# Kernel optimization log

Hardware: AMD Instinct MI355X
Metric: run time of the kernel (lower is better)

The kernel has to match this reference:

```python
import jax, jax.numpy as jnp
import numpy as np

B, L, D = 4, 2048, 512
H = 8
DK = 512 // H  # 64
DV = 512 // H  # 64
TEMP = float(np.power(DK, 0.5))
LN_EPS = 1e-5


def setup_inputs() -> dict:
    key = jax.random.key(0)
    ks = jax.random.split(key, 12)
    s = 0.02
    return {
        "q": jax.random.normal(ks[0], (B, L, D), jnp.float32),
        "k": jax.random.normal(ks[1], (B, L, D), jnp.float32),
        "v": jax.random.normal(ks[2], (B, L, D), jnp.float32),
        "mask": jax.random.randint(ks[3], (B, L, L), 0, 2, jnp.int32),
        "wq_w": jax.random.normal(ks[4], (H * DK, D), jnp.float32) * s,
        "wq_b": jnp.zeros((H * DK,), jnp.float32),
        "wv_w": jax.random.normal(ks[5], (H * DV, D), jnp.float32) * s,
        "wv_b": jnp.zeros((H * DV,), jnp.float32),
        "fc_w": jax.random.normal(ks[6], (D, H * DV), jnp.float32) * s,
        "fc_b": jnp.zeros((D,), jnp.float32),
        "ln_g": jnp.ones((D,), jnp.float32),
        "ln_b": jnp.zeros((D,), jnp.float32),
    }


def reference(q, k, v, mask, wq_w, wq_b, wv_w, wv_b, fc_w, fc_b, ln_g, ln_b):
    residual = q
    # NOTE: source module projects k with w_qs (bug preserved faithfully)
    qh = (q @ wq_w.T + wq_b).reshape(B, L, H, DK).transpose(0, 2, 1, 3)  # bhld
    kh = (k @ wq_w.T + wq_b).reshape(B, L, H, DK).transpose(0, 2, 1, 3)
    vh = (v @ wv_w.T + wv_b).reshape(B, L, H, DV).transpose(0, 2, 1, 3)
    attn = jnp.einsum("bhqd,bhkd->bhqk", qh / TEMP, kh)
    attn = jnp.where(mask[:, None, :, :] == 1, -1e9, attn)
    attn = jax.nn.softmax(attn, axis=-1)
    out = jnp.einsum("bhqk,bhkd->bhqd", attn, vh)  # (B, H, L, DV)
    # faithful buffer reinterpretation: .view(n_head, sz_b, L, DV)
    out = out.reshape(H, B, L, DV).transpose(0, 2, 1, 3).reshape(B, L, H * DV)
    out = out @ fc_w.T + fc_b
    x = out + residual
    mu = jnp.mean(x, axis=-1, keepdims=True)
    var = jnp.mean(jnp.square(x - mu), axis=-1, keepdims=True)
    y = (x - mu) / jnp.sqrt(var + LN_EPS) * ln_g + ln_b
    return (y, attn)
```

## Files before the change

kernel.cpp:

```cpp
#include <hip/hip_runtime.h>

#define NB 4
#define NL 2048
#define ND 512
#define NH 8
#define NTOK (NB * NL)

constexpr float LN_EPS = 1e-5f;

typedef __attribute__((ext_vector_type(8))) short bf16x8;
typedef __attribute__((ext_vector_type(4))) float f32x4;

static __device__ __forceinline__ unsigned short f2bf(float f) {
  unsigned u = __builtin_bit_cast(unsigned, f);
  unsigned r = (u + 0x7fffu + ((u >> 16) & 1u)) >> 16;
  return (unsigned short)r;
}

static __device__ __forceinline__ uint2 pk4(const float4 f) {
  uint2 r;
  r.x = (unsigned)f2bf(f.x) | ((unsigned)f2bf(f.y) << 16);
  r.y = (unsigned)f2bf(f.z) | ((unsigned)f2bf(f.w) << 16);
  return r;
}

__global__ __launch_bounds__(256) void cvt3_bf16(const float* __restrict__ s0,
                                                 const float* __restrict__ s1,
                                                 const float* __restrict__ s2,
                                                 unsigned short* __restrict__ d0,
                                                 unsigned short* __restrict__ d1,
                                                 unsigned short* __restrict__ d2) {
  const float* s = (blockIdx.y == 0) ? s0 : (blockIdx.y == 1) ? s1 : s2;
  unsigned short* d = (blockIdx.y == 0) ? d0 : (blockIdx.y == 1) ? d1 : d2;
  const size_t i = ((size_t)blockIdx.x * 256 + threadIdx.x) * 8;
  const float4 a = *(const float4*)&s[i];
  const float4 b = *(const float4*)&s[i + 4];
  uint4 o;
  const uint2 lo = pk4(a), hi = pk4(b);
  o.x = lo.x; o.y = lo.y; o.z = hi.x; o.w = hi.y;
  *(uint4*)&d[i] = o;
}

__global__ __launch_bounds__(256) void pack_mask(const int* __restrict__ mask,
                                                 unsigned long long* __restrict__ mpk) {
  const int w = threadIdx.x >> 6, lane = threadIdx.x & 63;
  const size_t g = (size_t)blockIdx.x * 4 + w;
  const int m = mask[g * 64 + lane];
  const unsigned long long bits = __ballot(m == 1);
  if (lane == 0) mpk[g] = bits;
}

#define BF16_GEMM_PRELUDE                                                      \
  __shared__ unsigned short As[64 * 72];                                       \
  __shared__ unsigned short Bs[64 * 72];                                       \
  const int tid = threadIdx.x;                                                 \
  const int w = tid >> 6;                                                      \
  const int lane = tid & 63;                                                   \
  const int quad = lane >> 4, l15 = lane & 15;                                 \
  const int m0 = blockIdx.x * 64, n0 = blockIdx.y * 64;                        \
  const int srow = tid >> 2;                                                   \
  const int scol = (tid & 3) * 16;                                             \
  f32x4 acc[4];                                                                \
  acc[0] = acc[1] = acc[2] = acc[3] = (f32x4){0.f, 0.f, 0.f, 0.f};

#define BF16_GEMM_STEP(ap, bp)                                                 \
  do {                                                                         \
    const uint4 a0 = *(const uint4*)((ap));                                    \
    const uint4 a1 = *(const uint4*)((ap) + 8);                                \
    const uint4 b0 = *(const uint4*)((bp));                                    \
    const uint4 b1 = *(const uint4*)((bp) + 8);                                \
    __syncthreads();                                                           \
    *(uint4*)&As[srow * 72 + scol] = a0;                                       \
    *(uint4*)&As[srow * 72 + scol + 8] = a1;                                   \
    *(uint4*)&Bs[srow * 72 + scol] = b0;                                       \
    *(uint4*)&Bs[srow * 72 + scol + 8] = b1;                                   \
    __syncthreads();                                                           \
    _Pragma("unroll") for (int ks = 0; ks < 2; ++ks) {                         \
      const bf16x8 af = *(const bf16x8*)&As[(w * 16 + l15) * 72 + ks * 32 + quad * 8]; \
      _Pragma("unroll") for (int nt = 0; nt < 4; ++nt) {                       \
        const bf16x8 bfr = *(const bf16x8*)&Bs[(nt * 16 + l15) * 72 + ks * 32 + quad * 8]; \
        acc[nt] = __builtin_amdgcn_mfma_f32_16x16x32_bf16(af, bfr, acc[nt], 0, 0, 0); \
      }                                                                        \
    }                                                                          \
  } while (0)

__global__ __launch_bounds__(256) void gemm_qk_mfma(const unsigned short* __restrict__ X,
                                                    const unsigned short* __restrict__ W,
                                                    const float* __restrict__ bias,
                                                    unsigned short* __restrict__ out,
                                                    float scale) {
  BF16_GEMM_PRELUDE
  for (int k0 = 0; k0 < 512; k0 += 64) {
    const unsigned short* ap = X + (size_t)(m0 + srow) * ND + k0 + scol;
    const unsigned short* bp = W + (size_t)(n0 + srow) * ND + k0 + scol;
    BF16_GEMM_STEP(ap, bp);
  }
  const int hh = n0 >> 6;
  __syncthreads();
#pragma unroll
  for (int nt = 0; nt < 4; ++nt) {
    const float b = bias[n0 + nt * 16 + l15];
#pragma unroll
    for (int r = 0; r < 4; ++r)
      As[(w * 16 + quad * 4 + r) * 72 + nt * 16 + l15] = f2bf((acc[nt][r] + b) * scale);
  }
  __syncthreads();
  const int tok = m0 + srow;
  const int bb = tok >> 11, l = tok & 2047;
  unsigned short* orow = out + (((size_t)bb * NH + hh) * NL + l) * 64;
  *(uint4*)&orow[scol] = *(const uint4*)&As[srow * 72 + scol];
  *(uint4*)&orow[scol + 8] = *(const uint4*)&As[srow * 72 + scol + 8];
}

__global__ __launch_bounds__(256) void gemm_v_mfma_t(const unsigned short* __restrict__ X,
                                                     const unsigned short* __restrict__ W,
                                                     const float* __restrict__ bias,
                                                     unsigned short* __restrict__ outT) {
  BF16_GEMM_PRELUDE
  for (int k0 = 0; k0 < 512; k0 += 64) {
    const unsigned short* ap = X + (size_t)(m0 + srow) * ND + k0 + scol;
    const unsigned short* bp = W + (size_t)(n0 + srow) * ND + k0 + scol;
    BF16_GEMM_STEP(ap, bp);
  }
  const int hh = n0 >> 6;
  __syncthreads();
#pragma unroll
  for (int nt = 0; nt < 4; ++nt) {
    const float b = bias[n0 + nt * 16 + l15];
#pragma unroll
    for (int r = 0; r < 4; ++r)
      As[(nt * 16 + l15) * 72 + w * 16 + quad * 4 + r] = f2bf(acc[nt][r] + b);
  }
  __syncthreads();
  const int bb = m0 >> 11, l0 = m0 & 2047;
  unsigned short* orow = outT + (((size_t)bb * NH + hh) * 64 + srow) * NL + l0;
  *(uint4*)&orow[scol] = *(const uint4*)&As[srow * 72 + scol];
  *(uint4*)&orow[scol + 8] = *(const uint4*)&As[srow * 72 + scol + 8];
}

__global__ __launch_bounds__(256) void attn_mfma(const unsigned short* __restrict__ qh,
                                                 const unsigned short* __restrict__ kh,
                                                 const unsigned short* __restrict__ vT,
                                                 const unsigned long long* __restrict__ mpk,
                                                 float* __restrict__ attn,
                                                 unsigned short* __restrict__ ao) {
  const int b = blockIdx.z, h = blockIdx.y, q0 = blockIdx.x * 64;
  const int bh = b * NH + h;
  __shared__ unsigned short Ks[64 * 72];
  __shared__ unsigned short Vt[64 * 72];
  __shared__ unsigned short Ps[4 * 16 * 72];
  const int tid = threadIdx.x;
  const int w = tid >> 6, lane = tid & 63;
  const int quad = lane >> 4, l15 = lane & 15;

  const size_t qoff = ((size_t)bh * NL + q0 + w * 16 + l15) * 64 + quad * 8;
  const bf16x8 aq0 = *(const bf16x8*)(qh + qoff);
  const bf16x8 aq1 = *(const bf16x8*)(qh + qoff + 32);

  const int srow = tid >> 2;
  const int scol = (tid & 3) * 16;

  const size_t mrowq = ((size_t)b * NL + q0 + w * 16 + quad * 4) * 32;

  float rinv[4] = {0.f, 0.f, 0.f, 0.f};
  unsigned int mbits[16];
#pragma unroll
  for (int i = 0; i < 16; ++i) mbits[i] = 0;

  for (int kt = 0; kt < 32; ++kt) {
    const unsigned short* kg = kh + ((size_t)bh * NL + kt * 64 + srow) * 64 + scol;
    const uint4 k0 = *(const uint4*)kg;
    const uint4 k1 = *(const uint4*)(kg + 8);
    unsigned long long mq[4];
#pragma unroll
    for (int r = 0; r < 4; ++r) mq[r] = mpk[mrowq + (size_t)r * 32 + kt];
    __syncthreads();
    *(uint4*)&Ks[srow * 72 + scol] = k0;
    *(uint4*)&Ks[srow * 72 + scol + 8] = k1;
    __syncthreads();
    f32x4 s[4];
#pragma unroll
    for (int nt = 0; nt < 4; ++nt) {
      const bf16x8 b0 = *(const bf16x8*)&Ks[(nt * 16 + l15) * 72 + quad * 8];
      const bf16x8 b1 = *(const bf16x8*)&Ks[(nt * 16 + l15) * 72 + 32 + quad * 8];
      f32x4 acc = {0.f, 0.f, 0.f, 0.f};
      acc = __builtin_amdgcn_mfma_f32_16x16x32_bf16(aq0, b0, acc, 0, 0, 0);
      acc = __builtin_amdgcn_mfma_f32_16x16x32_bf16(aq1, b1, acc, 0, 0, 0);
      s[nt] = acc;
    }
    unsigned int mb = 0;
#pragma unroll
    for (int r = 0; r < 4; ++r) {
      const unsigned long long t = mq[r] >> l15;
      mb |= ((unsigned)t & 1u) << (0 + r);
      mb |= (((unsigned)t >> 16) & 1u) << (4 + r);
      mb |= (((unsigned)(t >> 32)) & 1u) << (8 + r);
      mb |= (((unsigned)(t >> 48)) & 1u) << (12 + r);
    }
#pragma unroll
    for (int r = 0; r < 4; ++r) {
#pragma unroll
      for (int nt = 0; nt < 4; ++nt) {
        const float e = ((mb >> (nt * 4 + r)) & 1u) ? 0.f : __expf(s[nt][r]);
        rinv[r] += e;
      }
    }
    mbits[kt >> 1] |= mb << ((kt & 1) * 16);
  }
#pragma unroll
  for (int r = 0; r < 4; ++r) {
    float v = rinv[r];
    v += __shfl_xor(v, 1);
    v += __shfl_xor(v, 2);
    v += __shfl_xor(v, 4);
    v += __shfl_xor(v, 8);
    rinv[r] = 1.0f / v;
  }

  f32x4 oacc[4];
#pragma unroll
  for (int nt = 0; nt < 4; ++nt) oacc[nt] = (f32x4){0.f, 0.f, 0.f, 0.f};

  for (int kt = 0; kt < 32; ++kt) {
    const unsigned short* kg = kh + ((size_t)bh * NL + kt * 64 + srow) * 64 + scol;
    const unsigned short* vg = vT + ((size_t)bh * 64 + srow) * NL + kt * 64 + scol;
    const uint4 k0 = *(const uint4*)kg;
    const uint4 k1 = *(const uint4*)(kg + 8);
    const uint4 v0 = *(const uint4*)vg;
    const uint4 v1 = *(const uint4*)(vg + 8);
    __syncthreads();
    *(uint4*)&Ks[srow * 72 + scol] = k0;
    *(uint4*)&Ks[srow * 72 + scol + 8] = k1;
    *(uint4*)&Vt[srow * 72 + scol] = v0;
    *(uint4*)&Vt[srow * 72 + scol + 8] = v1;
    __syncthreads();
    f32x4 s[4];
#pragma unroll
    for (int nt = 0; nt < 4; ++nt) {
      const bf16x8 b0 = *(const bf16x8*)&Ks[(nt * 16 + l15) * 72 + quad * 8];
      const bf16x8 b1 = *(const bf16x8*)&Ks[(nt * 16 + l15) * 72 + 32 + quad * 8];
      f32x4 acc = {0.f, 0.f, 0.f, 0.f};
      acc = __builtin_amdgcn_mfma_f32_16x16x32_bf16(aq0, b0, acc, 0, 0, 0);
      acc = __builtin_amdgcn_mfma_f32_16x16x32_bf16(aq1, b1, acc, 0, 0, 0);
      s[nt] = acc;
    }
    const unsigned int mb = mbits[kt >> 1] >> ((kt & 1) * 16);
#pragma unroll
    for (int r = 0; r < 4; ++r) {
      const int q = q0 + w * 16 + quad * 4 + r;
      float* arow = attn + ((size_t)bh * NL + q) * NL + kt * 64;
      unsigned short* prow = &Ps[(w * 16 + quad * 4 + r) * 72];
#pragma unroll
      for (int nt = 0; nt < 4; ++nt) {
        float e = ((mb >> (nt * 4 + r)) & 1u) ? 0.f : __expf(s[nt][r]) * rinv[r];
        arow[nt * 16 + l15] = e;
        prow[nt * 16 + l15] = f2bf(e);
      }
    }
    const bf16x8 pa0 = *(const bf16x8*)&Ps[(w * 16 + l15) * 72 + quad * 8];
    const bf16x8 pa1 = *(const bf16x8*)&Ps[(w * 16 + l15) * 72 + 32 + quad * 8];
#pragma unroll
    for (int nt = 0; nt < 4; ++nt) {
      const bf16x8 vb0 = *(const bf16x8*)&Vt[(nt * 16 + l15) * 72 + quad * 8];
      const bf16x8 vb1 = *(const bf16x8*)&Vt[(nt * 16 + l15) * 72 + 32 + quad * 8];
      oacc[nt] = __builtin_amdgcn_mfma_f32_16x16x32_bf16(pa0, vb0, oacc[nt], 0, 0, 0);
      oacc[nt] = __builtin_amdgcn_mfma_f32_16x16x32_bf16(pa1, vb1, oacc[nt], 0, 0, 0);
    }
  }
#pragma unroll
  for (int nt = 0; nt < 4; ++nt)
#pragma unroll
    for (int r = 0; r < 4; ++r)
      Ps[(w * 16 + quad * 4 + r) * 72 + nt * 16 + l15] = f2bf(oacc[nt][r]);
  const int erow = lane >> 2;
  const int ecol = (lane & 3) * 16;
  unsigned short* orow = ao + (((size_t)bh * NL + q0 + w * 16 + erow) * 64) + ecol;
  *(uint4*)&orow[0] = *(const uint4*)&Ps[(w * 16 + erow) * 72 + ecol];
  *(uint4*)&orow[8] = *(const uint4*)&Ps[(w * 16 + erow) * 72 + ecol + 8];
}

__global__ __launch_bounds__(256) void fc_gather_mfma(const unsigned short* __restrict__ AO,
                                                      const unsigned short* __restrict__ W,
                                                      const float* __restrict__ bias,
                                                      const float* __restrict__ resid,
                                                      float* __restrict__ Xout) {
  BF16_GEMM_PRELUDE
  const int nrow = m0 + srow;
  const int b_out = nrow >> 11;
  const int l_out = nrow & 2047;
  const int h2 = b_out * 2 + (l_out >> 10);
  const int q2base = (l_out & 1023) << 1;
  for (int k0 = 0; k0 < 512; k0 += 64) {
    const int q2 = q2base | ((k0 >> 8) & 1);
    const int b2 = (k0 >> 6) & 3;
    const unsigned short* ap = AO + ((size_t)(h2 * 4 + b2) * NL + q2) * 64 + scol;
    const unsigned short* bp = W + (size_t)(n0 + srow) * ND + k0 + scol;
    BF16_GEMM_STEP(ap, bp);
  }
#pragma unroll
  for (int nt = 0; nt < 4; ++nt) {
    const float b = bias[n0 + nt * 16 + l15];
#pragma unroll
    for (int r = 0; r < 4; ++r) {
      const int row = m0 + w * 16 + quad * 4 + r;
      const float rv = resid[(size_t)row * ND + n0 + nt * 16 + l15];
      Xout[(size_t)row * ND + n0 + nt * 16 + l15] = acc[nt][r] + b + rv;
    }
  }
}

__global__ __launch_bounds__(64) void layernorm_k(const float* __restrict__ x,
                                                  const float* __restrict__ g,
                                                  const float* __restrict__ bta,
                                                  float* __restrict__ y) {
  const int n = blockIdx.x;
  const int lane = threadIdx.x;
  const float* row = x + (size_t)n * ND;
  const float4 a = *(const float4*)&row[lane * 8];
  const float4 c = *(const float4*)&row[lane * 8 + 4];
  float s = a.x + a.y + a.z + a.w + c.x + c.y + c.z + c.w;
  float sq = a.x * a.x + a.y * a.y + a.z * a.z + a.w * a.w +
             c.x * c.x + c.y * c.y + c.z * c.z + c.w * c.w;
#pragma unroll
  for (int off = 32; off; off >>= 1) {
    s += __shfl_down(s, off);
    sq += __shfl_down(sq, off);
  }
  s = __shfl(s, 0);
  sq = __shfl(sq, 0);
  const float mu = s * (1.f / 512.f);
  const float var = sq * (1.f / 512.f) - mu * mu;
  const float rstd = rsqrtf(var + LN_EPS);
  float* yo = y + (size_t)n * ND;
  const int c0 = lane * 8;
  float4 o1, o2;
  o1.x = (a.x - mu) * rstd * g[c0 + 0] + bta[c0 + 0];
  o1.y = (a.y - mu) * rstd * g[c0 + 1] + bta[c0 + 1];
  o1.z = (a.z - mu) * rstd * g[c0 + 2] + bta[c0 + 2];
  o1.w = (a.w - mu) * rstd * g[c0 + 3] + bta[c0 + 3];
  o2.x = (c.x - mu) * rstd * g[c0 + 4] + bta[c0 + 4];
  o2.y = (c.y - mu) * rstd * g[c0 + 5] + bta[c0 + 5];
  o2.z = (c.z - mu) * rstd * g[c0 + 6] + bta[c0 + 6];
  o2.w = (c.w - mu) * rstd * g[c0 + 7] + bta[c0 + 7];
  *(float4*)&yo[c0] = o1;
  *(float4*)&yo[c0 + 4] = o2;
}

extern "C" void kernel_launch(void* const* d_in, const int* in_sizes, int n_in,
                              void* d_out, int out_size, void* d_ws, size_t ws_size,
                              hipStream_t stream) {
  const float* q = (const float*)d_in[0];
  const float* k = (const float*)d_in[1];
  const float* v = (const float*)d_in[2];
  const int* mask = (const int*)d_in[3];
  const float* wq_w = (const float*)d_in[4];
  const float* wq_b = (const float*)d_in[5];
  const float* wv_w = (const float*)d_in[6];
  const float* wv_b = (const float*)d_in[7];
  const float* fc_w = (const float*)d_in[8];
  const float* fc_b = (const float*)d_in[9];
  const float* ln_g = (const float*)d_in[10];
  const float* ln_b = (const float*)d_in[11];

  float* y = (float*)d_out;
  float* attn = y + (size_t)NTOK * ND;

  const size_t SZ = (size_t)NTOK * ND;
  const size_t WSZ = (size_t)ND * ND;
  unsigned short* qhb = (unsigned short*)d_ws;
  unsigned short* khb = qhb + SZ;
  unsigned short* vTb = khb + SZ;
  unsigned short* aob = vTb + SZ;
  unsigned short* qb = aob + SZ;
  unsigned short* kb = qb + SZ;
  unsigned short* vb = kb + SZ;
  float* xx = (float*)(vb + SZ);
  unsigned short* wqb = (unsigned short*)(xx + SZ);
  unsigned short* wvb = wqb + WSZ;
  unsigned short* fcwb = wvb + WSZ;
  unsigned long long* mpk = (unsigned long long*)(fcwb + WSZ);

  cvt3_bf16<<<dim3(SZ / 2048, 3), 256, 0, stream>>>(q, k, v, qb, kb, vb);
  cvt3_bf16<<<dim3(WSZ / 2048, 3), 256, 0, stream>>>(wq_w, wv_w, fc_w, wqb, wvb, fcwb);
  pack_mask<<<(NB * NL * 32) / 4, 256, 0, stream>>>(mask, mpk);

  const dim3 gproj(NTOK / 64, ND / 64);
  gemm_qk_mfma<<<gproj, 256, 0, stream>>>(qb, wqb, wq_b, qhb, 0.125f);
  gemm_qk_mfma<<<gproj, 256, 0, stream>>>(kb, wqb, wq_b, khb, 1.0f);
  gemm_v_mfma_t<<<gproj, 256, 0, stream>>>(vb, wvb, wv_b, vTb);
  attn_mfma<<<dim3(NL / 64, NH, NB), 256, 0, stream>>>(qhb, khb, vTb, mpk, attn, aob);
  fc_gather_mfma<<<gproj, 256, 0, stream>>>(aob, fcwb, fc_b, q, xx);
  layernorm_k<<<NTOK, 64, 0, stream>>>(xx, ln_g, ln_b, y);
}
```

Baseline: 822.0 us.

## Double-buffer 128-row GEMM tiles, prefetch K/V in attention, use exp2

```diff
diff --git a/kernel.cpp b/kernel.cpp
--- a/kernel.cpp
+++ b/kernel.cpp
@@ -50,38 +50,49 @@
   if (lane == 0) mpk[g] = bits;
 }
 
-#define BF16_GEMM_PRELUDE                                                      \
-  __shared__ unsigned short As[64 * 72];                                       \
-  __shared__ unsigned short Bs[64 * 72];                                       \
+#define GEMM128_PRELUDE                                                        \
+  __shared__ unsigned short As[2][128 * 72];                                   \
+  __shared__ unsigned short Bs[2][64 * 72];                                    \
   const int tid = threadIdx.x;                                                 \
   const int w = tid >> 6;                                                      \
   const int lane = tid & 63;                                                   \
   const int quad = lane >> 4, l15 = lane & 15;                                 \
-  const int m0 = blockIdx.x * 64, n0 = blockIdx.y * 64;                        \
-  const int srow = tid >> 2;                                                   \
-  const int scol = (tid & 3) * 16;                                             \
-  f32x4 acc[4];                                                                \
-  acc[0] = acc[1] = acc[2] = acc[3] = (f32x4){0.f, 0.f, 0.f, 0.f};
-
-#define BF16_GEMM_STEP(ap, bp)                                                 \
-  do {                                                                         \
-    const uint4 a0 = *(const uint4*)((ap));                                    \
-    const uint4 a1 = *(const uint4*)((ap) + 8);                                \
-    const uint4 b0 = *(const uint4*)((bp));                                    \
-    const uint4 b1 = *(const uint4*)((bp) + 8);                                \
-    __syncthreads();                                                           \
-    *(uint4*)&As[srow * 72 + scol] = a0;                                       \
-    *(uint4*)&As[srow * 72 + scol + 8] = a1;                                   \
-    *(uint4*)&Bs[srow * 72 + scol] = b0;                                       \
-    *(uint4*)&Bs[srow * 72 + scol + 8] = b1;                                   \
-    __syncthreads();                                                           \
+  const int m0 = blockIdx.x * 128, n0 = blockIdx.y * 64;                       \
+  const int arow = tid >> 1;                                       \
+  const int acol = (tid & 1) * 32;                     \
+  const int brow = tid >> 2;                                        \
+  const int bcol = (tid & 3) * 16;                                             \
+  f32x4 acc[2][4];                                                             \
+  _Pragma("unroll") for (int mr = 0; mr < 2; ++mr)                             \
+  _Pragma("unroll") for (int nt = 0; nt < 4; ++nt)                             \
+    acc[mr][nt] = (f32x4){0.f, 0.f, 0.f, 0.f};                                 \
+  uint4 ar[4], br[2];
+
+#define GEMM128_STORE_LDS(buf)                                                 \
+  do {                                                                         \
+    _Pragma("unroll") for (int j = 0; j < 4; ++j)                              \
+      *(uint4*)&As[buf][arow * 72 + acol + j * 8] = ar[j];                     \
+    *(uint4*)&Bs[buf][brow * 72 + bcol] = br[0];                               \
+    *(uint4*)&Bs[buf][brow * 72 + bcol + 8] = br[1];                           \
+  } while (0)
+
+#define GEMM128_COMPUTE(buf)                                                   \
+  do {                                                                         \
     _Pragma("unroll") for (int ks = 0; ks < 2; ++ks) {                         \
-      const bf16x8 af = *(const bf16x8*)&As[(w * 16 + l15) * 72 + ks * 32 + quad * 8]; \
+      const bf16x8 af0 = *(const bf16x8*)&As[buf][(w * 32 + l15) * 72 + ks * 32 + quad * 8]; \
+      const bf16x8 af1 = *(const bf16x8*)&As[buf][(w * 32 + 16 + l15) * 72 + ks * 32 + quad * 8]; \
       _Pragma("unroll") for (int nt = 0; nt < 4; ++nt) {                       \
-        const bf16x8 bfr = *(const bf16x8*)&Bs[(nt * 16 + l15) * 72 + ks * 32 + quad * 8]; \
-        acc[nt] = __builtin_amdgcn_mfma_f32_16x16x32_bf16(af, bfr, acc[nt], 0, 0, 0); \
+        const bf16x8 bfr = *(const bf16x8*)&Bs[buf][(nt * 16 + l15) * 72 + ks * 32 + quad * 8]; \
+        acc[0][nt] = __builtin_amdgcn_mfma_f32_16x16x32_bf16(af0, bfr, acc[0][nt], 0, 0, 0); \
+        acc[1][nt] = __builtin_amdgcn_mfma_f32_16x16x32_bf16(af1, bfr, acc[1][nt], 0, 0, 0); \
       }                                                                        \
     }                                                                          \
+  } while (0)
+
+#define GEMM128_LOADB(k0)                                                      \
+  do {                                                                         \
+    br[0] = *(const uint4*)&W[(size_t)(n0 + brow) * ND + (k0) + bcol];         \
+    br[1] = *(const uint4*)&W[(size_t)(n0 + brow) * ND + (k0) + bcol + 8];     \
   } while (0)
 
 __global__ __launch_bounds__(256) void gemm_qk_mfma(const unsigned short* __restrict__ X,
@@ -89,53 +100,90 @@
                                                     const float* __restrict__ bias,
                                                     unsigned short* __restrict__ out,
                                                     float scale) {
-  BF16_GEMM_PRELUDE
-  for (int k0 = 0; k0 < 512; k0 += 64) {
-    const unsigned short* ap = X + (size_t)(m0 + srow) * ND + k0 + scol;
-    const unsigned short* bp = W + (size_t)(n0 + srow) * ND + k0 + scol;
-    BF16_GEMM_STEP(ap, bp);
-  }
+  GEMM128_PRELUDE
+#define LOADA_QK(k0)                                                           \
+  do {                                                                         \
+    _Pragma("unroll") for (int j = 0; j < 4; ++j)                              \
+      ar[j] = *(const uint4*)&X[(size_t)(m0 + arow) * ND + (k0) + acol + j * 8]; \
+  } while (0)
+  LOADA_QK(0);
+  GEMM128_LOADB(0);
+#pragma unroll
+  for (int t = 0; t < 8; ++t) {
+    const int buf = t & 1;
+    GEMM128_STORE_LDS(buf);
+    __syncthreads();
+    if (t < 7) {
+      LOADA_QK((t + 1) * 64);
+      GEMM128_LOADB((t + 1) * 64);
+    }
+    GEMM128_COMPUTE(buf);
+  }
+#undef LOADA_QK
   const int hh = n0 >> 6;
+#pragma unroll
+  for (int mr = 0; mr < 2; ++mr)
+#pragma unroll
+    for (int nt = 0; nt < 4; ++nt) {
+      const float b = bias[n0 + nt * 16 + l15];
+#pragma unroll
+      for (int r = 0; r < 4; ++r)
+        As[0][(w * 32 + mr * 16 + quad * 4 + r) * 72 + nt * 16 + l15] =
+            f2bf((acc[mr][nt][r] + b) * scale);
+    }
   __syncthreads();
-#pragma unroll
-  for (int nt = 0; nt < 4; ++nt) {
-    const float b = bias[n0 + nt * 16 + l15];
-#pragma unroll
-    for (int r = 0; r < 4; ++r)
-      As[(w * 16 + quad * 4 + r) * 72 + nt * 16 + l15] = f2bf((acc[nt][r] + b) * scale);
-  }
-  __syncthreads();
-  const int tok = m0 + srow;
+  const int tok = m0 + arow;
   const int bb = tok >> 11, l = tok & 2047;
   unsigned short* orow = out + (((size_t)bb * NH + hh) * NL + l) * 64;
-  *(uint4*)&orow[scol] = *(const uint4*)&As[srow * 72 + scol];
-  *(uint4*)&orow[scol + 8] = *(const uint4*)&As[srow * 72 + scol + 8];
+#pragma unroll
+  for (int j = 0; j < 4; ++j)
+    *(uint4*)&orow[acol + j * 8] = *(const uint4*)&As[0][arow * 72 + acol + j * 8];
 }
 
 __global__ __launch_bounds__(256) void gemm_v_mfma_t(const unsigned short* __restrict__ X,
                                                      const unsigned short* __restrict__ W,
                                                      const float* __restrict__ bias,
                                                      unsigned short* __restrict__ outT) {
-  BF16_GEMM_PRELUDE
-  for (int k0 = 0; k0 < 512; k0 += 64) {
-    const unsigned short* ap = X + (size_t)(m0 + srow) * ND + k0 + scol;
-    const unsigned short* bp = W + (size_t)(n0 + srow) * ND + k0 + scol;
-    BF16_GEMM_STEP(ap, bp);
-  }
+  GEMM128_PRELUDE
+#define LOADA_V(k0)                                                            \
+  do {                                                                         \
+    _Pragma("unroll") for (int j = 0; j < 4; ++j)                              \
+      ar[j] = *(const uint4*)&X[(size_t)(m0 + arow) * ND + (k0) + acol + j * 8]; \
+  } while (0)
+  LOADA_V(0);
+  GEMM128_LOADB(0);
+#pragma unroll
+  for (int t = 0; t < 8; ++t) {
+    const int buf = t & 1;
+    GEMM128_STORE_LDS(buf);
+    __syncthreads();
+    if (t < 7) {
+      LOADA_V((t + 1) * 64);
+      GEMM128_LOADB((t + 1) * 64);
+    }
+    GEMM128_COMPUTE(buf);
+  }
+#undef LOADA_V
   const int hh = n0 >> 6;
-  __syncthreads();
-#pragma unroll
-  for (int nt = 0; nt < 4; ++nt) {
-    const float b = bias[n0 + nt * 16 + l15];
-#pragma unroll
-    for (int r = 0; r < 4; ++r)
-      As[(nt * 16 + l15) * 72 + w * 16 + quad * 4 + r] = f2bf(acc[nt][r] + b);
-  }
+  unsigned short* T = &As[0][0];
+#pragma unroll
+  for (int mr = 0; mr < 2; ++mr)
+#pragma unroll
+    for (int nt = 0; nt < 4; ++nt) {
+      const float b = bias[n0 + nt * 16 + l15];
+#pragma unroll
+      for (int r = 0; r < 4; ++r)
+        T[(nt * 16 + l15) * 136 + (w * 32 + mr * 16 + quad * 4 + r)] =
+            f2bf(acc[mr][nt][r] + b);
+    }
   __syncthreads();
   const int bb = m0 >> 11, l0 = m0 & 2047;
-  unsigned short* orow = outT + (((size_t)bb * NH + hh) * 64 + srow) * NL + l0;
-  *(uint4*)&orow[scol] = *(const uint4*)&As[srow * 72 + scol];
-  *(uint4*)&orow[scol + 8] = *(const uint4*)&As[srow * 72 + scol + 8];
+  const int d = tid >> 2;
+  const int lcol = (tid & 3) * 32;
+  unsigned short* orow = outT + (((size_t)bb * NH + hh) * 64 + d) * NL + l0;
+#pragma unroll
+  for (int j = 0; j < 4; ++j)
+    *(uint4*)&orow[lcol + j * 8] = *(const uint4*)&T[d * 136 + lcol + j * 8];
 }
 
 __global__ __launch_bounds__(256) void attn_mfma(const unsigned short* __restrict__ qh,
@@ -160,52 +208,58 @@
   const int srow = tid >> 2;
   const int scol = (tid & 3) * 16;
 
+  const size_t kbase = ((size_t)bh * NL + srow) * 64 + scol;
+  const size_t vbase = ((size_t)bh * 64 + srow) * NL + scol;
   const size_t mrowq = ((size_t)b * NL + q0 + w * 16 + quad * 4) * 32;
 
   float rinv[4] = {0.f, 0.f, 0.f, 0.f};
-  unsigned int mbits[16];
-#pragma unroll
-  for (int i = 0; i < 16; ++i) mbits[i] = 0;
-
-  for (int kt = 0; kt < 32; ++kt) {
-    const unsigned short* kg = kh + ((size_t)bh * NL + kt * 64 + srow) * 64 + scol;
-    const uint4 k0 = *(const uint4*)kg;
-    const uint4 k1 = *(const uint4*)(kg + 8);
-    unsigned long long mq[4];
-#pragma unroll
-    for (int r = 0; r < 4; ++r) mq[r] = mpk[mrowq + (size_t)r * 32 + kt];
-    __syncthreads();
-    *(uint4*)&Ks[srow * 72 + scol] = k0;
-    *(uint4*)&Ks[srow * 72 + scol + 8] = k1;
-    __syncthreads();
-    f32x4 s[4];
-#pragma unroll
-    for (int nt = 0; nt < 4; ++nt) {
-      const bf16x8 b0 = *(const bf16x8*)&Ks[(nt * 16 + l15) * 72 + quad * 8];
-      const bf16x8 b1 = *(const bf16x8*)&Ks[(nt * 16 + l15) * 72 + 32 + quad * 8];
-      f32x4 acc = {0.f, 0.f, 0.f, 0.f};
-      acc = __builtin_amdgcn_mfma_f32_16x16x32_bf16(aq0, b0, acc, 0, 0, 0);
-      acc = __builtin_amdgcn_mfma_f32_16x16x32_bf16(aq1, b1, acc, 0, 0, 0);
-      s[nt] = acc;
-    }
-    unsigned int mb = 0;
-#pragma unroll
-    for (int r = 0; r < 4; ++r) {
-      const unsigned long long t = mq[r] >> l15;
-      mb |= ((unsigned)t & 1u) << (0 + r);
-      mb |= (((unsigned)t >> 16) & 1u) << (4 + r);
-      mb |= (((unsigned)(t >> 32)) & 1u) << (8 + r);
-      mb |= (((unsigned)(t >> 48)) & 1u) << (12 + r);
-    }
-#pragma unroll
-    for (int r = 0; r < 4; ++r) {
+
+  {
+    uint4 kr0 = *(const uint4*)(kh + kbase);
+    uint4 kr1 = *(const uint4*)(kh + kbase + 8);
+    unsigned long long mqr[4];
+#pragma unroll
+    for (int r = 0; r < 4; ++r) mqr[r] = mpk[mrowq + (size_t)r * 32];
+
+    for (int kt = 0; kt < 32; ++kt) {
+      __syncthreads();
+      *(uint4*)&Ks[srow * 72 + scol] = kr0;
+      *(uint4*)&Ks[srow * 72 + scol + 8] = kr1;
+      __syncthreads();
+      unsigned int mb = 0;
+#pragma unroll
+      for (int r = 0; r < 4; ++r) {
+        const unsigned long long t = mqr[r] >> l15;
+        mb |= ((unsigned)t & 1u) << (0 + r);
+        mb |= (((unsigned)t >> 16) & 1u) << (4 + r);
+        mb |= (((unsigned)(t >> 32)) & 1u) << (8 + r);
+        mb |= (((unsigned)(t >> 48)) & 1u) << (12 + r);
+      }
+      if (kt < 31) {
+        const size_t kb2 = kbase + (size_t)(kt + 1) * 64 * 64;
+        kr0 = *(const uint4*)(kh + kb2);
+        kr1 = *(const uint4*)(kh + kb2 + 8);
+#pragma unroll
+        for (int r = 0; r < 4; ++r) mqr[r] = mpk[mrowq + (size_t)r * 32 + kt + 1];
+      }
+      f32x4 s[4];
 #pragma unroll
       for (int nt = 0; nt < 4; ++nt) {
-        const float e = ((mb >> (nt * 4 + r)) & 1u) ? 0.f : __expf(s[nt][r]);
-        rinv[r] += e;
-      }
-    }
-    mbits[kt >> 1] |= mb << ((kt & 1) * 16);
+        const bf16x8 b0 = *(const bf16x8*)&Ks[(nt * 16 + l15) * 72 + quad * 8];
+        const bf16x8 b1 = *(const bf16x8*)&Ks[(nt * 16 + l15) * 72 + 32 + quad * 8];
+        f32x4 a2 = {0.f, 0.f, 0.f, 0.f};
+        a2 = __builtin_amdgcn_mfma_f32_16x16x32_bf16(aq0, b0, a2, 0, 0, 0);
+        a2 = __builtin_amdgcn_mfma_f32_16x16x32_bf16(aq1, b1, a2, 0, 0, 0);
+        s[nt] = a2;
+      }
+#pragma unroll
+      for (int r = 0; r < 4; ++r)
+#pragma unroll
+        for (int nt = 0; nt < 4; ++nt) {
+          const float e = ((mb >> (nt * 4 + r)) & 1u) ? 0.f : exp2f(s[nt][r]);
+          rinv[r] += e;
+        }
+    }
   }
 #pragma unroll
   for (int r = 0; r < 4; ++r) {
@@ -221,50 +275,72 @@
 #pragma unroll
   for (int nt = 0; nt < 4; ++nt) oacc[nt] = (f32x4){0.f, 0.f, 0.f, 0.f};
 
-  for (int kt = 0; kt < 32; ++kt) {
-    const unsigned short* kg = kh + ((size_t)bh * NL + kt * 64 + srow) * 64 + scol;
-    const unsigned short* vg = vT + ((size_t)bh * 64 + srow) * NL + kt * 64 + scol;
-    const uint4 k0 = *(const uint4*)kg;
-    const uint4 k1 = *(const uint4*)(kg + 8);
-    const uint4 v0 = *(const uint4*)vg;
-    const uint4 v1 = *(const uint4*)(vg + 8);
-    __syncthreads();
-    *(uint4*)&Ks[srow * 72 + scol] = k0;
-    *(uint4*)&Ks[srow * 72 + scol + 8] = k1;
-    *(uint4*)&Vt[srow * 72 + scol] = v0;
-    *(uint4*)&Vt[srow * 72 + scol + 8] = v1;
-    __syncthreads();
-    f32x4 s[4];
-#pragma unroll
-    for (int nt = 0; nt < 4; ++nt) {
-      const bf16x8 b0 = *(const bf16x8*)&Ks[(nt * 16 + l15) * 72 + quad * 8];
-      const bf16x8 b1 = *(const bf16x8*)&Ks[(nt * 16 + l15) * 72 + 32 + quad * 8];
-      f32x4 acc = {0.f, 0.f, 0.f, 0.f};
-      acc = __builtin_amdgcn_mfma_f32_16x16x32_bf16(aq0, b0, acc, 0, 0, 0);
-      acc = __builtin_amdgcn_mfma_f32_16x16x32_bf16(aq1, b1, acc, 0, 0, 0);
-      s[nt] = acc;
-    }
-    const unsigned int mb = mbits[kt >> 1] >> ((kt & 1) * 16);
-#pragma unroll
-    for (int r = 0; r < 4; ++r) {
-      const int q = q0 + w * 16 + quad * 4 + r;
-      float* arow = attn + ((size_t)bh * NL + q) * NL + kt * 64;
-      unsigned short* prow = &Ps[(w * 16 + quad * 4 + r) * 72];
+  {
+    uint4 kr0 = *(const uint4*)(kh + kbase);
+    uint4 kr1 = *(const uint4*)(kh + kbase + 8);
+    uint4 vr0 = *(const uint4*)(vT + vbase);
+    uint4 vr1 = *(const uint4*)(vT + vbase + 8);
+    unsigned long long mqr[4];
+#pragma unroll
+    for (int r = 0; r < 4; ++r) mqr[r] = mpk[mrowq + (size_t)r * 32];
+
+    for (int kt = 0; kt < 32; ++kt) {
+      __syncthreads();
+      *(uint4*)&Ks[srow * 72 + scol] = kr0;
+      *(uint4*)&Ks[srow * 72 + scol + 8] = kr1;
+      *(uint4*)&Vt[srow * 72 + scol] = vr0;
+      *(uint4*)&Vt[srow * 72 + scol + 8] = vr1;
+      __syncthreads();
+      unsigned int mb = 0;
+#pragma unroll
+      for (int r = 0; r < 4; ++r) {
+        const unsigned long long t = mqr[r] >> l15;
+        mb |= ((unsigned)t & 1u) << (0 + r);
+        mb |= (((unsigned)t >> 16) & 1u) << (4 + r);
+        mb |= (((unsigned)(t >> 32)) & 1u) << (8 + r);
+        mb |= (((unsigned)(t >> 48)) & 1u) << (12 + r);
+      }
+      if (kt < 31) {
+        const size_t kb2 = kbase + (size_t)(kt + 1) * 64 * 64;
+        const size_t vb2 = vbase + (size_t)(kt + 1) * 64;
+        kr0 = *(const uint4*)(kh + kb2);
+        kr1 = *(const uint4*)(kh + kb2 + 8);
+        vr0 = *(const uint4*)(vT + vb2);
+        vr1 = *(const uint4*)(vT + vb2 + 8);
+#pragma unroll
+        for (int r = 0; r < 4; ++r) mqr[r] = mpk[mrowq + (size_t)r * 32 + kt + 1];
+      }
+      f32x4 s[4];
 #pragma unroll
       for (int nt = 0; nt < 4; ++nt) {
-        float e = ((mb >> (nt * 4 + r)) & 1u) ? 0.f : __expf(s[nt][r]) * rinv[r];
-        arow[nt * 16 + l15] = e;
-        prow[nt * 16 + l15] = f2bf(e);
-      }
-    }
-    const bf16x8 pa0 = *(const bf16x8*)&Ps[(w * 16 + l15) * 72 + quad * 8];
-    const bf16x8 pa1 = *(const bf16x8*)&Ps[(w * 16 + l15) * 72 + 32 + quad * 8];
-#pragma unroll
-    for (int nt = 0; nt < 4; ++nt) {
-      const bf16x8 vb0 = *(const bf16x8*)&Vt[(nt * 16 + l15) * 72 + quad * 8];
-      const bf16x8 vb1 = *(const bf16x8*)&Vt[(nt * 16 + l15) * 72 + 32 + quad * 8];
-      oacc[nt] = __builtin_amdgcn_mfma_f32_16x16x32_bf16(pa0, vb0, oacc[nt], 0, 0, 0);
-      oacc[nt] = __builtin_amdgcn_mfma_f32_16x16x32_bf16(pa1, vb1, oacc[nt], 0, 0, 0);
+        const bf16x8 b0 = *(const bf16x8*)&Ks[(nt * 16 + l15) * 72 + quad * 8];
+        const bf16x8 b1 = *(const bf16x8*)&Ks[(nt * 16 + l15) * 72 + 32 + quad * 8];
+        f32x4 a2 = {0.f, 0.f, 0.f, 0.f};
+        a2 = __builtin_amdgcn_mfma_f32_16x16x32_bf16(aq0, b0, a2, 0, 0, 0);
+        a2 = __builtin_amdgcn_mfma_f32_16x16x32_bf16(aq1, b1, a2, 0, 0, 0);
+        s[nt] = a2;
+      }
+#pragma unroll
+      for (int r = 0; r < 4; ++r) {
+        const int q = q0 + w * 16 + quad * 4 + r;
+        float* arow = attn + ((size_t)bh * NL + q) * NL + kt * 64;
+        unsigned short* prow = &Ps[(w * 16 + quad * 4 + r) * 72];
+#pragma unroll
+        for (int nt = 0; nt < 4; ++nt) {
+          float e = ((mb >> (nt * 4 + r)) & 1u) ? 0.f : exp2f(s[nt][r]) * rinv[r];
+          arow[nt * 16 + l15] = e;
+          prow[nt * 16 + l15] = f2bf(e);
+        }
+      }
+      const bf16x8 pa0 = *(const bf16x8*)&Ps[(w * 16 + l15) * 72 + quad * 8];
+      const bf16x8 pa1 = *(const bf16x8*)&Ps[(w * 16 + l15) * 72 + 32 + quad * 8];
+#pragma unroll
+      for (int nt = 0; nt < 4; ++nt) {
+        const bf16x8 vb0 = *(const bf16x8*)&Vt[(nt * 16 + l15) * 72 + quad * 8];
+        const bf16x8 vb1 = *(const bf16x8*)&Vt[(nt * 16 + l15) * 72 + 32 + quad * 8];
+        oacc[nt] = __builtin_amdgcn_mfma_f32_16x16x32_bf16(pa0, vb0, oacc[nt], 0, 0, 0);
+        oacc[nt] = __builtin_amdgcn_mfma_f32_16x16x32_bf16(pa1, vb1, oacc[nt], 0, 0, 0);
+      }
     }
   }
 #pragma unroll
@@ -284,37 +360,55 @@
                                                       const float* __restrict__ bias,
                                                       const float* __restrict__ resid,
                                                       float* __restrict__ Xout) {
-  BF16_GEMM_PRELUDE
-  const int nrow = m0 + srow;
+  GEMM128_PRELUDE
+  const int nrow = m0 + arow;
   const int b_out = nrow >> 11;
   const int l_out = nrow & 2047;
   const int h2 = b_out * 2 + (l_out >> 10);
   const int q2base = (l_out & 1023) << 1;
-  for (int k0 = 0; k0 < 512; k0 += 64) {
-    const int q2 = q2base | ((k0 >> 8) & 1);
-    const int b2 = (k0 >> 6) & 3;
-    const unsigned short* ap = AO + ((size_t)(h2 * 4 + b2) * NL + q2) * 64 + scol;
-    const unsigned short* bp = W + (size_t)(n0 + srow) * ND + k0 + scol;
-    BF16_GEMM_STEP(ap, bp);
-  }
-#pragma unroll
-  for (int nt = 0; nt < 4; ++nt) {
-    const float b = bias[n0 + nt * 16 + l15];
-#pragma unroll
-    for (int r = 0; r < 4; ++r) {
-      const int row = m0 + w * 16 + quad * 4 + r;
-      const float rv = resid[(size_t)row * ND + n0 + nt * 16 + l15];
-      Xout[(size_t)row * ND + n0 + nt * 16 + l15] = acc[nt][r] + b + rv;
-    }
-  }
-}
-
-__global__ __launch_bounds__(64) void layernorm_k(const float* __restrict__ x,
-                                                  const float* __restrict__ g,
-                                                  const float* __restrict__ bta,
-                                                  float* __restrict__ y) {
-  const int n = blockIdx.x;
-  const int lane = threadIdx.x;
+#define LOADA_FC(k0)                                                           \
+  do {                                                                         \
+    const int q2 = q2base | (((k0) >> 8) & 1);                                 \
+    const int b2 = ((k0) >> 6) & 3;                                            \
+    const unsigned short* abase = AO + ((size_t)(h2 * 4 + b2) * NL + q2) * 64; \
+    _Pragma("unroll") for (int j = 0; j < 4; ++j)                              \
+      ar[j] = *(const uint4*)&abase[acol + j * 8];                             \
+  } while (0)
+  LOADA_FC(0);
+  GEMM128_LOADB(0);
+#pragma unroll
+  for (int t = 0; t < 8; ++t) {
+    const int buf = t & 1;
+    GEMM128_STORE_LDS(buf);
+    __syncthreads();
+    if (t < 7) {
+      LOADA_FC((t + 1) * 64);
+      GEMM128_LOADB((t + 1) * 64);
+    }
+    GEMM128_COMPUTE(buf);
+  }
+#undef LOADA_FC
+#pragma unroll
+  for (int mr = 0; mr < 2; ++mr)
+#pragma unroll
+    for (int nt = 0; nt < 4; ++nt) {
+      const float b = bias[n0 + nt * 16 + l15];
+#pragma unroll
+      for (int r = 0; r < 4; ++r) {
+        const int row = m0 + w * 32 + mr * 16 + quad * 4 + r;
+        const int col = n0 + nt * 16 + l15;
+        const float rv = resid[(size_t)row * ND + col];
+        Xout[(size_t)row * ND + col] = acc[mr][nt][r] + b + rv;
+      }
+    }
+}
+
+__global__ __launch_bounds__(256) void layernorm_k(const float* __restrict__ x,
+                                                   const float* __restrict__ g,
+                                                   const float* __restrict__ bta,
+                                                   float* __restrict__ y) {
+  const int n = blockIdx.x * 4 + (threadIdx.x >> 6);
+  const int lane = threadIdx.x & 63;
   const float* row = x + (size_t)n * ND;
   const float4 a = *(const float4*)&row[lane * 8];
   const float4 c = *(const float4*)&row[lane * 8 + 4];
@@ -384,11 +478,11 @@
   cvt3_bf16<<<dim3(WSZ / 2048, 3), 256, 0, stream>>>(wq_w, wv_w, fc_w, wqb, wvb, fcwb);
   pack_mask<<<(NB * NL * 32) / 4, 256, 0, stream>>>(mask, mpk);
 
-  const dim3 gproj(NTOK / 64, ND / 64);
-  gemm_qk_mfma<<<gproj, 256, 0, stream>>>(qb, wqb, wq_b, qhb, 0.125f);
+  const dim3 gproj(NTOK / 128, ND / 64);
+  gemm_qk_mfma<<<gproj, 256, 0, stream>>>(qb, wqb, wq_b, qhb, 0.125f * 1.44269504f);
   gemm_qk_mfma<<<gproj, 256, 0, stream>>>(kb, wqb, wq_b, khb, 1.0f);
   gemm_v_mfma_t<<<gproj, 256, 0, stream>>>(vb, wvb, wv_b, vTb);
   attn_mfma<<<dim3(NL / 64, NH, NB), 256, 0, stream>>>(qhb, khb, vTb, mpk, attn, aob);
   fc_gather_mfma<<<gproj, 256, 0, stream>>>(aob, fcwb, fc_b, q, xx);
-  layernorm_k<<<NTOK, 64, 0, stream>>>(xx, ln_g, ln_b, y);
-}
+  layernorm_k<<<NTOK / 4, 256, 0, stream>>>(xx, ln_g, ln_b, y);
+}
```

Result: slower. 849.5 us (+3.4%).
